# Optimization experiments

Measured on AMD Instinct MI355X. Metric: run time of the kernel, lower is better.

Reference implementation:

```python
import math
import jax, jax.numpy as jnp
import numpy as np

NUM_HEADS = 16
NEG_INF = -1e30


def setup_inputs() -> dict:
    key = jax.random.key(0)
    k1, k2, k3, k4 = jax.random.split(key, 4)
    B, C, T = 4, 1024, 2048
    x = jax.random.normal(k1, (B, C, T), dtype=jnp.float32)
    mask = jax.random.randint(k2, (B, T), 0, 2, dtype=jnp.int32)
    # kernel-size-1 Conv1d with bias=False == matmul; torch init scale ~ 1/sqrt(fan_in)
    W_mem = jax.random.normal(k3, (2 * C, C), dtype=jnp.float32) / math.sqrt(C)
    W_q = jax.random.normal(k4, (C, C), dtype=jnp.float32) / math.sqrt(C)
    return {"x": x, "mask": mask, "W_mem": W_mem, "W_q": W_q}


def reference(x, mask, W_mem, W_q):
    B, C, T = x.shape
    nh = NUM_HEADS
    dh = C // nh
    # kernel-size-1 conv projections, output already transposed to [B, T, ch]
    memory = jnp.einsum('oc,bct->bto', W_mem, x)   # [B, T, 2C]
    query = jnp.einsum('oc,bct->bto', W_q, x)      # [B, T, C]
    Q = query.reshape(B, T, nh, dh).transpose(0, 2, 1, 3)           # [B, nh, T, dh]
    Km, Vm = jnp.split(memory, 2, axis=-1)
    K = Km.reshape(B, T, nh, dh).transpose(0, 2, 1, 3)              # [B, nh, T, dh]
    V = Vm.reshape(B, T, nh, dh).transpose(0, 2, 1, 3)              # [B, nh, T, dh]
    att = jnp.einsum('bhqd,bhkd->bhqk', Q, K) * (1.0 / math.sqrt(dh))
    m = mask.reshape(B, 1, 1, T).astype(att.dtype)
    logits = m * att + (1.0 - m) * NEG_INF  # masked_softmax convention
    weights = jax.nn.softmax(logits, axis=-1)
    # dropout is identity in eval mode
    out = jnp.einsum('bhqk,bhkd->bhqd', weights, V)                 # [B, nh, T, dh]
    return out.transpose(0, 2, 1, 3).reshape(B, T, C).transpose(0, 2, 1)  # [B, C, T]
```

## Files before the change

kernel.cpp:

```cpp
#include <hip/hip_runtime.h>

#define B_ 4
#define C_ 1024
#define T_ 2048
#define NH 16
#define DH 64
#define TC 3072

typedef __attribute__((ext_vector_type(8))) short short8;
typedef __attribute__((ext_vector_type(4))) short short4v;
typedef __attribute__((ext_vector_type(4))) float f32x4;
typedef __attribute__((ext_vector_type(16))) float f32x16;
typedef __attribute__((ext_vector_type(2))) unsigned int u32x2;
typedef __attribute__((ext_vector_type(4))) unsigned int u32x4;

#define S2Q 0.1803368801111204f

static __device__ __forceinline__ unsigned short f2bf(float f){
  unsigned int u = __builtin_bit_cast(unsigned int, f);
  u += 0x7fffu + ((u >> 16) & 1u);
  return (unsigned short)(u >> 16);
}

__global__ __launch_bounds__(256) void cast_w_kernel(const float* __restrict__ Wmem,
                                                     const float* __restrict__ Wq,
                                                     unsigned short* __restrict__ Wc){
  size_t base = ((size_t)blockIdx.x*256 + threadIdx.x)*4;
  float4 v;
  if (base < (size_t)2048*1024) v = *(const float4*)(Wmem + base);
  else                          v = *(const float4*)(Wq + (base - (size_t)2048*1024));
  short4v o;
  o.x = (short)f2bf(v.x); o.y = (short)f2bf(v.y);
  o.z = (short)f2bf(v.z); o.w = (short)f2bf(v.w);
  *(short4v*)(Wc + base) = o;
}

__global__ __launch_bounds__(256) void scan_mask_kernel(const int* __restrict__ mask,
    int* __restrict__ idx, int* __restrict__ nkinfo, float* __restrict__ cbias){
  __shared__ int cnt[256];
  int b = blockIdx.x;
  int tid = threadIdx.x;
  const int* mb = mask + (size_t)b*T_;
  int base = tid*8;
  int m[8]; int c = 0;
  #pragma unroll
  for (int i=0;i<8;i++){ m[i] = mb[base+i]; c += m[i]; }
  cnt[tid] = c;
  __syncthreads();
  for (int off=1; off<256; off<<=1){
    int v = (tid >= off) ? cnt[tid-off] : 0;
    __syncthreads();
    cnt[tid] += v;
    __syncthreads();
  }
  int nk  = cnt[255];
  int pos = cnt[tid] - c;
  #pragma unroll
  for (int i=0;i<8;i++){
    if (m[i]) idx[(size_t)b*T_ + (pos++)] = base + i;
  }
  #pragma unroll
  for (int i=0;i<8;i++){
    int j = base + i;
    cbias[(size_t)b*T_ + j] = (j < nk) ? 0.f : -1e30f;
  }
  if (tid == 0){
    nkinfo[b]   = (nk + 127) & ~127;
    nkinfo[4+b] = nk;
  }
}

__global__ __launch_bounds__(256) void transpose_x_kernel(const float* __restrict__ x,
                                                          unsigned short* __restrict__ xT){
  __shared__ float tile[32][33];
  int b = blockIdx.z;
  int c0 = blockIdx.y*32, t0 = blockIdx.x*32;
  int tx = threadIdx.x, ty = threadIdx.y;
  const float* xp = x + ((size_t)b*C_ + c0)*T_ + t0;
  #pragma unroll
  for (int i=0;i<4;i++) tile[ty+8*i][tx] = xp[(size_t)(ty+8*i)*T_ + tx];
  __syncthreads();
  unsigned short* op = xT + ((size_t)b*T_ + t0)*C_ + c0;
  int cp = tx & 15, tw = tx >> 4;
  #pragma unroll
  for (int i=0;i<2;i++){
    int trow = ty + 8*tw + 16*i;
    unsigned int pk = (unsigned int)f2bf(tile[2*cp][trow])
                    | ((unsigned int)f2bf(tile[2*cp+1][trow]) << 16);
    *(unsigned int*)(op + (size_t)trow*C_ + 2*cp) = pk;
  }
}

#define PBM 128
#define PBN 128
#define PBK 64

__global__ __launch_bounds__(256) void proj_gemm_kernel(const unsigned short* __restrict__ Wc,
    const unsigned short* __restrict__ xT, const int* __restrict__ idx,
    const int* __restrict__ nkinfo,
    unsigned short* __restrict__ Kb, unsigned short* __restrict__ Vt,
    unsigned short* __restrict__ Qb){
  __shared__ unsigned short sA[PBM*PBK];
  __shared__ unsigned short sB[PBN*PBK];
  int b = blockIdx.y;
  int d = blockIdx.x;
  int xcd = d & 7, j = d >> 3;
  int oq = xcd >> 1, th = xcd & 1;
  int o0 = (oq*6 + (j % 6)) * PBM;
  int t0 = ((j/6)*2 + th) * PBN;
  const bool isKV = (o0 < 2*C_);
  const int nk128 = nkinfo[b], nk = nkinfo[4+b];
  if (isKV && t0 >= nk128) return;
  int tid = threadIdx.x;
  int lane = tid & 63, wave = tid >> 6;
  int wr = wave >> 1, wc = wave & 1;
  f32x4 acc[4][4] = {};
  const unsigned short* Abase = Wc + (size_t)o0*C_;
  const unsigned short* xTb = xT + (size_t)b*T_*C_;
  auto ldsA = (__attribute__((address_space(3))) char*)sA;
  auto ldsB = (__attribute__((address_space(3))) char*)sB;
  const char* srcBrow[4];
  #pragma unroll
  for (int i=0;i<4;i++){
    int L  = wave*4096 + i*1024;
    int Ll = L + lane*16;
    int row = Ll >> 7;
    int jb  = Ll & 127;
    int trow = t0 + row;
    int grow = trow;
    if (isKV) grow = (trow < nk) ? idx[(size_t)b*T_ + trow] : 0;
    srcBrow[i] = (const char*)(xTb + (size_t)grow*C_) + jb;
  }
  for (int k0=0; k0<C_; k0+=PBK){
    #pragma unroll
    for (int i=0;i<4;i++){
      int L  = wave*4096 + i*1024;
      int Ll = L + lane*16;
      int row = Ll >> 7;
      int jb  = Ll & 127;
      const char* srcA = (const char*)(Abase + (size_t)row*C_ + k0) + jb;
      const char* srcB = srcBrow[i] + (size_t)k0*2;
      __builtin_amdgcn_global_load_lds((const __attribute__((address_space(1))) void*)srcA,
                                       (__attribute__((address_space(3))) void*)(ldsA + L), 16, 0, 0);
      __builtin_amdgcn_global_load_lds((const __attribute__((address_space(1))) void*)srcB,
                                       (__attribute__((address_space(3))) void*)(ldsB + L), 16, 0, 0);
    }
    __syncthreads();
    #pragma unroll
    for (int ks=0; ks<2; ks++){
      short8 af[4], bfr[4];
      #pragma unroll
      for (int m=0;m<4;m++){
        int row = wr*64 + m*16 + (lane & 15);
        af[m] = *(const short8*)((const char*)sA + row*128 + ks*64 + ((lane>>4)*16));
      }
      #pragma unroll
      for (int n=0;n<4;n++){
        int row = wc*64 + n*16 + (lane & 15);
        bfr[n] = *(const short8*)((const char*)sB + row*128 + ks*64 + ((lane>>4)*16));
      }
      #pragma unroll
      for (int m=0;m<4;m++){
        #pragma unroll
        for (int n=0;n<4;n++)
          acc[m][n] = __builtin_amdgcn_mfma_f32_16x16x32_bf16(af[m], bfr[n], acc[m][n], 0, 0, 0);
      }
    }
    __syncthreads();
  }
  int rowbase = o0 + wr*64;
  #pragma unroll
  for (int m=0;m<4;m++){
    int o = rowbase + m*16 + ((lane>>4)*4);
    #pragma unroll
    for (int n=0;n<4;n++){
      int t = t0 + wc*64 + n*16 + (lane & 15);
      f32x4 v = acc[m][n];
      if (o < C_){
        int h = o >> 6, dd = o & 63;
        unsigned short* p = Kb + (((size_t)(b*NH + h)*T_ + t)*DH + dd);
        short4v s; s.x=(short)f2bf(v.x); s.y=(short)f2bf(v.y);
        s.z=(short)f2bf(v.z); s.w=(short)f2bf(v.w);
        *(short4v*)p = s;
      } else if (o < 2*C_){
        int oo = o - C_;
        int h = oo >> 6, dd = oo & 63;
        unsigned short* p = Vt + (((size_t)(b*NH + h)*DH + dd)*T_ + t);
        p[0]    = f2bf(v.x);
        p[T_]   = f2bf(v.y);
        p[2*T_] = f2bf(v.z);
        p[3*T_] = f2bf(v.w);
      } else {
        int oo = o - 2*C_;
        int h = oo >> 6, dd = oo & 63;
        unsigned short* p = Qb + (((size_t)(b*NH + h)*T_ + t)*DH + dd);
        short4v s; s.x=(short)f2bf(v.x*S2Q); s.y=(short)f2bf(v.y*S2Q);
        s.z=(short)f2bf(v.z*S2Q); s.w=(short)f2bf(v.w*S2Q);
        *(short4v*)p = s;
      }
    }
  }
}

#define KB_ 64

#define GLL(SRC, SHBUF, LOFF) \
  __builtin_amdgcn_global_load_lds((const __attribute__((address_space(1))) void*)(SRC), \
      (__attribute__((address_space(3))) void*)((__attribute__((address_space(3))) char*)(SHBUF) + (LOFF)), 16, 0, 0)

#define MAX3(a,b,c) fmaxf(fmaxf((a),(b)),(c))

__global__ __launch_bounds__(256) void attn_kernel(const unsigned short* __restrict__ Qb,
    const unsigned short* __restrict__ Kb, const unsigned short* __restrict__ Vt,
    const float* __restrict__ cbias, const int* __restrict__ nkinfo,
    float* __restrict__ out){
  __shared__ unsigned short sK[2][KB_*DH];
  __shared__ unsigned short sV[2][KB_*DH];
  const int Lid = blockIdx.x;
  const int xcd = Lid & 7, jj = Lid >> 3;
  const int bh = ((jj & 7) << 3) | xcd;
  const int qblk = jj >> 3;
  const int b = bh >> 4;
  const int ntiles = nkinfo[b] >> 6;
  const int tid = threadIdx.x, lane = tid & 63, wave = tid >> 6;
  const int l31 = lane & 31, h = lane >> 5;
  const int rsw = l31 & 7;
  const unsigned short* Kbase = Kb + (size_t)bh*T_*DH;
  const unsigned short* Vbase = Vt + (size_t)bh*DH*T_;
  const float* bptr = cbias + (size_t)b*T_ + 4*h;
  const int qrow = qblk*128 + wave*32 + l31;
  const unsigned short* Qp = Qb + ((size_t)bh*T_ + qrow)*DH + h*8;
  short8 qf[4];
  #pragma unroll
  for (int kc=0;kc<4;kc++) qf[kc] = *(const short8*)(Qp + kc*16);
  f32x16 acco0 = {}, acco1 = {};
  float mrun = -1e30f, lpart = 0.f;
  const int L0  = wave*2048;
  const int Ll0 = L0 + lane*16, Ll1 = Ll0 + 1024;
  const int row0 = Ll0 >> 7, row1 = Ll1 >> 7;
  const int cg0 = ((Ll0 >> 4) & 7) ^ (row0 & 7);
  const int cg1 = ((Ll1 >> 4) & 7) ^ (row1 & 7);
  const char* srcK0 = (const char*)Kbase + row0*128 + cg0*16;
  const char* srcK1 = (const char*)Kbase + row1*128 + cg1*16;
  const char* srcV0 = (const char*)Vbase + (size_t)row0*(T_*2) + cg0*16;
  const char* srcV1 = (const char*)Vbase + (size_t)row1*(T_*2) + cg1*16;

  GLL(srcK0, &sK[0][0], L0);
  GLL(srcK1, &sK[0][0], L0 + 1024);
  GLL(srcV0, &sV[0][0], L0);
  GLL(srcV1, &sV[0][0], L0 + 1024);
  srcK0 += 8192; srcK1 += 8192; srcV0 += 128; srcV1 += 128;
  __syncthreads();

  for (int kt = 0; kt < ntiles; kt++){
    const int cb = kt & 1;
    union { f32x4 q[4]; f32x16 v; } cb0, cb1;
    #pragma unroll
    for (int m=0;m<4;m++){
      cb0.q[m] = *(const f32x4*)(bptr + m*8);
      cb1.q[m] = *(const f32x4*)(bptr + 32 + m*8);
    }
    bptr += 64;
    if (kt + 1 < ntiles){
      int db = cb ^ 1;
      GLL(srcK0, &sK[0][0], db*8192 + L0);
      GLL(srcK1, &sK[0][0], db*8192 + L0 + 1024);
      GLL(srcV0, &sV[0][0], db*8192 + L0);
      GLL(srcV1, &sV[0][0], db*8192 + L0 + 1024);
      srcK0 += 8192; srcK1 += 8192; srcV0 += 128; srcV1 += 128;
      asm volatile("s_waitcnt vmcnt(12)" ::: "memory");
    } else {
      asm volatile("s_waitcnt vmcnt(8)" ::: "memory");
    }
    __builtin_amdgcn_s_barrier();
    __builtin_amdgcn_sched_barrier(0);
    const char* sKb = (const char*)&sK[0][0] + cb*8192 + l31*128;
    const char* sVb = (const char*)&sV[0][0] + cb*8192 + l31*128;
    f32x16 s0 = cb0.v, s1 = cb1.v;
    #pragma unroll
    for (int kc=0;kc<4;kc++){
      int co = (((kc<<1)|h) ^ rsw) << 4;
      short8 kf0 = *(const short8*)(sKb + co);
      short8 kf1 = *(const short8*)(sKb + 4096 + co);
      s0 = __builtin_amdgcn_mfma_f32_32x32x16_bf16(kf0, qf[kc], s0, 0,0,0);
      s1 = __builtin_amdgcn_mfma_f32_32x32x16_bf16(kf1, qf[kc], s1, 0,0,0);
    }
    float t0_ = MAX3(s0[0],s0[1],s0[2]),   t1_ = MAX3(s0[3],s0[4],s0[5]);
    float t2_ = MAX3(s0[6],s0[7],s0[8]),   t3_ = MAX3(s0[9],s0[10],s0[11]);
    float t4_ = MAX3(s0[12],s0[13],s0[14]), t5_ = MAX3(s0[15],s1[0],s1[1]);
    float t6_ = MAX3(s1[2],s1[3],s1[4]),   t7_ = MAX3(s1[5],s1[6],s1[7]);
    float t8_ = MAX3(s1[8],s1[9],s1[10]),  t9_ = MAX3(s1[11],s1[12],s1[13]);
    float u0_ = MAX3(t0_,t1_,t2_), u1_ = MAX3(t3_,t4_,t5_);
    float u2_ = MAX3(t6_,t7_,t8_), u3_ = MAX3(t9_,s1[14],s1[15]);
    float pmax = MAX3(MAX3(u0_,u1_,u2_), u3_, -1e30f);
    if (!__all(pmax - mrun <= 8.0f)){
      float pm = fmaxf(pmax, __shfl_xor(pmax, 32));
      float mnew = fmaxf(mrun, pm);
      float alpha = __builtin_amdgcn_exp2f(mrun - mnew);
      mrun = mnew; lpart *= alpha;
      #pragma unroll
      for (int r=0;r<16;r++){
        float ar = __shfl(alpha, (r&3) + 8*(r>>2) + 4*h);
        acco0[r] *= ar; acco1[r] *= ar;
      }
    }
    float ps_ = 0.f;
    #pragma unroll
    for (int j=0;j<16;j++){
      s0[j] = __builtin_amdgcn_exp2f(s0[j] - mrun); ps_ += s0[j];
      s1[j] = __builtin_amdgcn_exp2f(s1[j] - mrun); ps_ += s1[j];
    }
    lpart += ps_;
    unsigned int Wp[2][4][2];
    #pragma unroll
    for (int m=0;m<4;m++){
      asm volatile("v_cvt_pk_bf16_f32 %0, %1, %2" : "=v"(Wp[0][m][0]) : "v"(s0[4*m]),   "v"(s0[4*m+1]));
      asm volatile("v_cvt_pk_bf16_f32 %0, %1, %2" : "=v"(Wp[0][m][1]) : "v"(s0[4*m+2]), "v"(s0[4*m+3]));
      asm volatile("v_cvt_pk_bf16_f32 %0, %1, %2" : "=v"(Wp[1][m][0]) : "v"(s1[4*m]),   "v"(s1[4*m+1]));
      asm volatile("v_cvt_pk_bf16_f32 %0, %1, %2" : "=v"(Wp[1][m][1]) : "v"(s1[4*m+2]), "v"(s1[4*m+3]));
    }
    #pragma unroll
    for (int kb=0;kb<2;kb++){
      #pragma unroll
      for (int e=0;e<2;e++){
        u32x2 x0 = __builtin_amdgcn_permlane32_swap(Wp[kb][2*e][0], Wp[kb][2*e+1][0], 0, 0);
        u32x2 x1 = __builtin_amdgcn_permlane32_swap(Wp[kb][2*e][1], Wp[kb][2*e+1][1], 0, 0);
        u32x4 pw; pw.x = x0.x; pw.y = x1.x; pw.z = x0.y; pw.w = x1.y;
        short8 pf = __builtin_bit_cast(short8, pw);
        int vo = (((((kb<<1)|e)<<1)|h) ^ rsw) << 4;
        short8 vf0 = *(const short8*)(sVb + vo);
        short8 vf1 = *(const short8*)(sVb + 4096 + vo);
        acco0 = __builtin_amdgcn_mfma_f32_32x32x16_bf16(pf, vf0, acco0, 0,0,0);
        acco1 = __builtin_amdgcn_mfma_f32_32x32x16_bf16(pf, vf1, acco1, 0,0,0);
      }
    }
    __builtin_amdgcn_sched_barrier(0);
    __builtin_amdgcn_s_barrier();
  }

  lpart += __shfl_xor(lpart, 32);
  float inv = 1.0f / lpart;
  const int head = bh & 15;
  const int qbase = qblk*128 + wave*32;
  #pragma unroll
  for (int m=0;m<4;m++){
    float rv[4];
    #pragma unroll
    for (int s=0;s<4;s++) rv[s] = __shfl(inv, 8*m + 4*h + s);
    int t = qbase + 8*m + 4*h;
    float4 v0, v1;
    v0.x = acco0[4*m+0]*rv[0]; v0.y = acco0[4*m+1]*rv[1];
    v0.z = acco0[4*m+2]*rv[2]; v0.w = acco0[4*m+3]*rv[3];
    v1.x = acco1[4*m+0]*rv[0]; v1.y = acco1[4*m+1]*rv[1];
    v1.z = acco1[4*m+2]*rv[2]; v1.w = acco1[4*m+3]*rv[3];
    size_t off0 = ((size_t)b*C_ + head*64 + l31)*T_ + t;
    size_t off1 = ((size_t)b*C_ + head*64 + 32 + l31)*T_ + t;
    *(float4*)(out + off0) = v0;
    *(float4*)(out + off1) = v1;
  }
}

extern "C" void kernel_launch(void* const* d_in, const int* in_sizes, int n_in,
                              void* d_out, int out_size, void* d_ws, size_t ws_size,
                              hipStream_t stream) {
  const float* x    = (const float*)d_in[0];
  const int*   mask = (const int*)d_in[1];
  const float* Wmem = (const float*)d_in[2];
  const float* Wq   = (const float*)d_in[3];
  float* out = (float*)d_out;

  unsigned short* ws = (unsigned short*)d_ws;
  unsigned short* xT = ws;
  unsigned short* Wc = xT + (size_t)B_*T_*C_;
  unsigned short* Qb = Wc + (size_t)TC*C_;
  unsigned short* Kb = Qb + (size_t)B_*NH*T_*DH;
  unsigned short* Vt = Kb + (size_t)B_*NH*T_*DH;
  float* cbias = (float*)(Vt + (size_t)B_*NH*T_*DH);
  int*   idx   = (int*)(cbias + (size_t)B_*T_);
  int*   nkinfo = idx + (size_t)B_*T_;

  cast_w_kernel<<<dim3(TC*C_/1024), dim3(256), 0, stream>>>(Wmem, Wq, Wc);
  scan_mask_kernel<<<dim3(B_), dim3(256), 0, stream>>>(mask, idx, nkinfo, cbias);
  transpose_x_kernel<<<dim3(T_/32, C_/32, B_), dim3(32,8), 0, stream>>>(x, xT);
  proj_gemm_kernel<<<dim3((TC/PBM)*(T_/PBN), B_), dim3(256), 0, stream>>>(Wc, xT, idx, nkinfo, Kb, Vt, Qb);
  attn_kernel<<<dim3((T_/128)*(B_*NH)), dim3(256), 0, stream>>>(Qb, Kb, Vt, cbias, nkinfo, out);
}
```

Baseline: 165.6 us.

## Double-buffer LDS tiles in projection GEMM to overlap loads with MFMA

The projection GEMM now uses two LDS buffers for the A and B tiles. It issues async global-to-LDS loads for the next K slice before computing on the current one, using a manual vmcnt wait and raw barriers in place of the two __syncthreads per iteration. This is meant to hide global memory latency behind MFMA work. In exchange, LDS use doubles to 64KB per block, which may lower occupancy, and correctness now depends on the hand-written waitcnt count.

```diff
diff --git a/kernel.cpp b/kernel.cpp
--- a/kernel.cpp
+++ b/kernel.cpp
@@ -100,8 +100,8 @@
     const int* __restrict__ nkinfo,
     unsigned short* __restrict__ Kb, unsigned short* __restrict__ Vt,
     unsigned short* __restrict__ Qb){
-  __shared__ unsigned short sA[PBM*PBK];
-  __shared__ unsigned short sB[PBN*PBK];
+  __shared__ unsigned short sA[2][PBM*PBK];
+  __shared__ unsigned short sB[2][PBN*PBK];
   int b = blockIdx.y;
   int d = blockIdx.x;
   int xcd = d & 7, j = d >> 3;
@@ -117,47 +117,63 @@
   f32x4 acc[4][4] = {};
   const unsigned short* Abase = Wc + (size_t)o0*C_;
   const unsigned short* xTb = xT + (size_t)b*T_*C_;
-  auto ldsA = (__attribute__((address_space(3))) char*)sA;
-  auto ldsB = (__attribute__((address_space(3))) char*)sB;
+  auto ldsA = (__attribute__((address_space(3))) char*)&sA[0][0];
+  auto ldsB = (__attribute__((address_space(3))) char*)&sB[0][0];
+  const int L  = wave*4096;
+  const int Ll = L + lane*16;
+  const int srow = Ll >> 7;
+  const int sjb  = Ll & 127;
   const char* srcBrow[4];
+  const char* srcArow[4];
   #pragma unroll
   for (int i=0;i<4;i++){
-    int L  = wave*4096 + i*1024;
-    int Ll = L + lane*16;
-    int row = Ll >> 7;
-    int jb  = Ll & 127;
+    int row = srow + i*8;
     int trow = t0 + row;
     int grow = trow;
     if (isKV) grow = (trow < nk) ? idx[(size_t)b*T_ + trow] : 0;
-    srcBrow[i] = (const char*)(xTb + (size_t)grow*C_) + jb;
-  }
-  for (int k0=0; k0<C_; k0+=PBK){
-    #pragma unroll
-    for (int i=0;i<4;i++){
-      int L  = wave*4096 + i*1024;
-      int Ll = L + lane*16;
-      int row = Ll >> 7;
-      int jb  = Ll & 127;
-      const char* srcA = (const char*)(Abase + (size_t)row*C_ + k0) + jb;
-      const char* srcB = srcBrow[i] + (size_t)k0*2;
-      __builtin_amdgcn_global_load_lds((const __attribute__((address_space(1))) void*)srcA,
-                                       (__attribute__((address_space(3))) void*)(ldsA + L), 16, 0, 0);
-      __builtin_amdgcn_global_load_lds((const __attribute__((address_space(1))) void*)srcB,
-                                       (__attribute__((address_space(3))) void*)(ldsB + L), 16, 0, 0);
-    }
-    __syncthreads();
+    srcBrow[i] = (const char*)(xTb + (size_t)grow*C_) + sjb;
+    srcArow[i] = (const char*)(Abase + (size_t)row*C_) + sjb;
+  }
+
+#define PSTAGE(BF, K0) do {                                                            \
+    _Pragma("unroll")                                                                  \
+    for (int i=0;i<4;i++){                                                             \
+      __builtin_amdgcn_global_load_lds(                                                \
+        (const __attribute__((address_space(1))) void*)(srcArow[i] + (size_t)(K0)*2),  \
+        (__attribute__((address_space(3))) void*)(ldsA + (BF)*16384 + L + i*1024), 16, 0, 0); \
+      __builtin_amdgcn_global_load_lds(                                                \
+        (const __attribute__((address_space(1))) void*)(srcBrow[i] + (size_t)(K0)*2),  \
+        (__attribute__((address_space(3))) void*)(ldsB + (BF)*16384 + L + i*1024), 16, 0, 0); \
+    }                                                                                  \
+  } while(0)
+
+  PSTAGE(0, 0);
+  __syncthreads();
+
+  for (int kk=0; kk<C_/PBK; kk++){
+    int bf = kk & 1;
+    if (kk + 1 < C_/PBK){
+      PSTAGE(bf^1, (kk+1)*PBK);
+      asm volatile("s_waitcnt vmcnt(8)" ::: "memory");
+    } else {
+      asm volatile("s_waitcnt vmcnt(0)" ::: "memory");
+    }
+    __builtin_amdgcn_s_barrier();
+    __builtin_amdgcn_sched_barrier(0);
+    const char* sAb = (const char*)&sA[bf][0];
+    const char* sBb = (const char*)&sB[bf][0];
     #pragma unroll
     for (int ks=0; ks<2; ks++){
       short8 af[4], bfr[4];
       #pragma unroll
       for (int m=0;m<4;m++){
         int row = wr*64 + m*16 + (lane & 15);
-        af[m] = *(const short8*)((const char*)sA + row*128 + ks*64 + ((lane>>4)*16));
+        af[m] = *(const short8*)(sAb + row*128 + ks*64 + ((lane>>4)*16));
       }
       #pragma unroll
       for (int n=0;n<4;n++){
         int row = wc*64 + n*16 + (lane & 15);
-        bfr[n] = *(const short8*)((const char*)sB + row*128 + ks*64 + ((lane>>4)*16));
+        bfr[n] = *(const short8*)(sBb + row*128 + ks*64 + ((lane>>4)*16));
       }
       #pragma unroll
       for (int m=0;m<4;m++){
@@ -166,8 +182,11 @@
           acc[m][n] = __builtin_amdgcn_mfma_f32_16x16x32_bf16(af[m], bfr[n], acc[m][n], 0, 0, 0);
       }
     }
-    __syncthreads();
-  }
+    __builtin_amdgcn_sched_barrier(0);
+    __builtin_amdgcn_s_barrier();
+  }
+#undef PSTAGE
+
   int rowbase = o0 + wr*64;
   #pragma unroll
   for (int m=0;m<4;m++){
```

Measured after the change: 165.8 us. No clear change (+0.1%).

## Project all K/V rows densely, then compact unmasked keys in a separate kernel

Applied to the files above, without the earlier changes.

The projection GEMM no longer gathers unmasked time rows through an index array and no longer skips tiles past the unmasked count. It computes K and V for every position. A new kernel then gathers the unmasked rows into compacted K/V buffers for attention. This gives simpler, contiguous GEMM loads in exchange for roughly double the K/V GEMM work, an extra launch, and scattered scalar gathers for the transposed V.

```diff
diff --git a/kernel.cpp b/kernel.cpp
--- a/kernel.cpp
+++ b/kernel.cpp
@@ -96,8 +96,7 @@
 #define PBK 64
 
 __global__ __launch_bounds__(256) void proj_gemm_kernel(const unsigned short* __restrict__ Wc,
-    const unsigned short* __restrict__ xT, const int* __restrict__ idx,
-    const int* __restrict__ nkinfo,
+    const unsigned short* __restrict__ xT,
     unsigned short* __restrict__ Kb, unsigned short* __restrict__ Vt,
     unsigned short* __restrict__ Qb){
   __shared__ unsigned short sA[PBM*PBK];
@@ -108,29 +107,14 @@
   int oq = xcd >> 1, th = xcd & 1;
   int o0 = (oq*6 + (j % 6)) * PBM;
   int t0 = ((j/6)*2 + th) * PBN;
-  const bool isKV = (o0 < 2*C_);
-  const int nk128 = nkinfo[b], nk = nkinfo[4+b];
-  if (isKV && t0 >= nk128) return;
   int tid = threadIdx.x;
   int lane = tid & 63, wave = tid >> 6;
   int wr = wave >> 1, wc = wave & 1;
   f32x4 acc[4][4] = {};
   const unsigned short* Abase = Wc + (size_t)o0*C_;
-  const unsigned short* xTb = xT + (size_t)b*T_*C_;
+  const unsigned short* Bbase = xT + ((size_t)b*T_ + t0)*C_;
   auto ldsA = (__attribute__((address_space(3))) char*)sA;
   auto ldsB = (__attribute__((address_space(3))) char*)sB;
-  const char* srcBrow[4];
-  #pragma unroll
-  for (int i=0;i<4;i++){
-    int L  = wave*4096 + i*1024;
-    int Ll = L + lane*16;
-    int row = Ll >> 7;
-    int jb  = Ll & 127;
-    int trow = t0 + row;
-    int grow = trow;
-    if (isKV) grow = (trow < nk) ? idx[(size_t)b*T_ + trow] : 0;
-    srcBrow[i] = (const char*)(xTb + (size_t)grow*C_) + jb;
-  }
   for (int k0=0; k0<C_; k0+=PBK){
     #pragma unroll
     for (int i=0;i<4;i++){
@@ -139,7 +123,7 @@
       int row = Ll >> 7;
       int jb  = Ll & 127;
       const char* srcA = (const char*)(Abase + (size_t)row*C_ + k0) + jb;
-      const char* srcB = srcBrow[i] + (size_t)k0*2;
+      const char* srcB = (const char*)(Bbase + (size_t)row*C_ + k0) + jb;
       __builtin_amdgcn_global_load_lds((const __attribute__((address_space(1))) void*)srcA,
                                        (__attribute__((address_space(3))) void*)(ldsA + L), 16, 0, 0);
       __builtin_amdgcn_global_load_lds((const __attribute__((address_space(1))) void*)srcB,
@@ -202,6 +186,49 @@
   }
 }
 
+__global__ __launch_bounds__(256) void compact_kv_kernel(const unsigned short* __restrict__ KbF,
+    const unsigned short* __restrict__ VtF, const int* __restrict__ idx,
+    const int* __restrict__ nkinfo,
+    unsigned short* __restrict__ Kc, unsigned short* __restrict__ Vc){
+  int bh = blockIdx.y;
+  int b = bh >> 4;
+  int nk128 = nkinfo[b], nk = nkinfo[4+b];
+  int tid = threadIdx.x;
+  int row = blockIdx.x*32 + (tid >> 3);
+  if (row < nk128){
+    int col = (tid & 7)*8;
+    const unsigned short* s;
+    short8 v;
+    if (row < nk){
+      int g = idx[(size_t)b*T_ + row];
+      v = *(const short8*)(KbF + ((size_t)bh*T_ + g)*DH + col);
+    } else {
+      v = short8{};
+    }
+    *(short8*)(Kc + ((size_t)bh*T_ + row)*DH + col) = v;
+  }
+  for (int it=0; it<2; it++){
+    int dd = blockIdx.x;
+    if (dd < DH){
+      int jj = (tid + it*256)*4;
+      if (jj < nk128){
+        short4v v;
+        #pragma unroll
+        for (int u=0;u<4;u++){
+          int j2 = jj + u;
+          unsigned short val = 0;
+          if (j2 < nk){
+            int g = idx[(size_t)b*T_ + j2];
+            val = VtF[((size_t)bh*DH + dd)*T_ + g];
+          }
+          ((unsigned short*)&v)[u] = val;
+        }
+        *(short4v*)(Vc + ((size_t)bh*DH + dd)*T_ + jj) = v;
+      }
+    }
+  }
+}
+
 #define KB_ 64
 
 #define GLL(SRC, SHBUF, LOFF) \
@@ -378,10 +405,13 @@
   float* cbias = (float*)(Vt + (size_t)B_*NH*T_*DH);
   int*   idx   = (int*)(cbias + (size_t)B_*T_);
   int*   nkinfo = idx + (size_t)B_*T_;
+  unsigned short* Kc = (unsigned short*)(nkinfo + 8);
+  unsigned short* Vc = Kc + (size_t)B_*NH*T_*DH;
 
   cast_w_kernel<<<dim3(TC*C_/1024), dim3(256), 0, stream>>>(Wmem, Wq, Wc);
   scan_mask_kernel<<<dim3(B_), dim3(256), 0, stream>>>(mask, idx, nkinfo, cbias);
   transpose_x_kernel<<<dim3(T_/32, C_/32, B_), dim3(32,8), 0, stream>>>(x, xT);
-  proj_gemm_kernel<<<dim3((TC/PBM)*(T_/PBN), B_), dim3(256), 0, stream>>>(Wc, xT, idx, nkinfo, Kb, Vt, Qb);
-  attn_kernel<<<dim3((T_/128)*(B_*NH)), dim3(256), 0, stream>>>(Qb, Kb, Vt, cbias, nkinfo, out);
-}
+  proj_gemm_kernel<<<dim3((TC/PBM)*(T_/PBN), B_), dim3(256), 0, stream>>>(Wc, xT, Kb, Vt, Qb);
+  compact_kv_kernel<<<dim3(T_/32, B_*NH), dim3(256), 0, stream>>>(Kb, Vt, idx, nkinfo, Kc, Vc);
+  attn_kernel<<<dim3((T_/128)*(B_*NH)), dim3(256), 0, stream>>>(Qb, Kc, Vc, cbias, nkinfo, out);
+}
```

Result: slower. 179.4 us (+8.3%).

## Use persistent 256x128 projection GEMM tiles with 512 threads and compacted tile list

Applied to the files above, without the earlier changes.

The projection GEMM switches to a persistent grid of 128 blocks per batch with 512 threads, each looping over a compacted list of 256x128 output tiles. Only Q tiles and the key/value tiles below the masked key count are visited. The change aims to cut grid-launch waste from early-exit blocks and to raise operand reuse per loaded B tile. The trade-off is larger LDS use per block, fewer resident blocks, and possible load imbalance across the persistent loop. The XCD-aware tile swizzle is removed.

```diff
diff --git a/kernel.cpp b/kernel.cpp
--- a/kernel.cpp
+++ b/kernel.cpp
@@ -91,114 +91,118 @@
   }
 }
 
-#define PBM 128
+#define PBM 256
 #define PBN 128
 #define PBK 64
 
-__global__ __launch_bounds__(256) void proj_gemm_kernel(const unsigned short* __restrict__ Wc,
+__global__ __launch_bounds__(512) void proj_gemm_kernel(const unsigned short* __restrict__ Wc,
     const unsigned short* __restrict__ xT, const int* __restrict__ idx,
     const int* __restrict__ nkinfo,
     unsigned short* __restrict__ Kb, unsigned short* __restrict__ Vt,
     unsigned short* __restrict__ Qb){
   __shared__ unsigned short sA[PBM*PBK];
   __shared__ unsigned short sB[PBN*PBK];
-  int b = blockIdx.y;
-  int d = blockIdx.x;
-  int xcd = d & 7, j = d >> 3;
-  int oq = xcd >> 1, th = xcd & 1;
-  int o0 = (oq*6 + (j % 6)) * PBM;
-  int t0 = ((j/6)*2 + th) * PBN;
-  const bool isKV = (o0 < 2*C_);
+  const int b = blockIdx.y;
+  const int d = blockIdx.x;
   const int nk128 = nkinfo[b], nk = nkinfo[4+b];
-  if (isKV && t0 >= nk128) return;
-  int tid = threadIdx.x;
-  int lane = tid & 63, wave = tid >> 6;
-  int wr = wave >> 1, wc = wave & 1;
-  f32x4 acc[4][4] = {};
-  const unsigned short* Abase = Wc + (size_t)o0*C_;
+  const int L = 64 + 8*(nk128 >> 7);
+  const int tid = threadIdx.x;
+  const int lane = tid & 63, wave = tid >> 6;
+  const int wr = wave >> 1, wc = wave & 1;
   const unsigned short* xTb = xT + (size_t)b*T_*C_;
   auto ldsA = (__attribute__((address_space(3))) char*)sA;
   auto ldsB = (__attribute__((address_space(3))) char*)sB;
-  const char* srcBrow[4];
-  #pragma unroll
-  for (int i=0;i<4;i++){
-    int L  = wave*4096 + i*1024;
-    int Ll = L + lane*16;
-    int row = Ll >> 7;
-    int jb  = Ll & 127;
-    int trow = t0 + row;
-    int grow = trow;
-    if (isKV) grow = (trow < nk) ? idx[(size_t)b*T_ + trow] : 0;
-    srcBrow[i] = (const char*)(xTb + (size_t)grow*C_) + jb;
-  }
-  for (int k0=0; k0<C_; k0+=PBK){
-    #pragma unroll
-    for (int i=0;i<4;i++){
-      int L  = wave*4096 + i*1024;
-      int Ll = L + lane*16;
-      int row = Ll >> 7;
-      int jb  = Ll & 127;
-      const char* srcA = (const char*)(Abase + (size_t)row*C_ + k0) + jb;
-      const char* srcB = srcBrow[i] + (size_t)k0*2;
-      __builtin_amdgcn_global_load_lds((const __attribute__((address_space(1))) void*)srcA,
-                                       (__attribute__((address_space(3))) void*)(ldsA + L), 16, 0, 0);
-      __builtin_amdgcn_global_load_lds((const __attribute__((address_space(1))) void*)srcB,
-                                       (__attribute__((address_space(3))) void*)(ldsB + L), 16, 0, 0);
+  const int l15 = lane & 15, lg4 = (lane >> 4)*16;
+
+  for (int i = d; i < L; i += 128){
+    int o0, t0;
+    bool isKV;
+    if (i < 64){ o0 = 2048 + (i >> 4)*PBM; t0 = (i & 15)*PBN; isKV = false; }
+    else       { int k = i - 64; o0 = (k & 7)*PBM; t0 = (k >> 3)*PBN; isKV = true; }
+    const unsigned short* Abase = Wc + (size_t)o0*C_;
+    f32x4 acc[4][4] = {};
+    const char* srcBrow[2];
+    #pragma unroll
+    for (int i2=0;i2<2;i2++){
+      int Ll = wave*2048 + i2*1024 + lane*16;
+      int row = Ll >> 7, jb = Ll & 127;
+      int t = t0 + row;
+      int grow = isKV ? ((t < nk) ? idx[(size_t)b*T_ + t] : 0) : t;
+      srcBrow[i2] = (const char*)(xTb + (size_t)grow*C_) + jb;
+    }
+    for (int k0=0; k0<C_; k0+=PBK){
+      #pragma unroll
+      for (int i2=0;i2<4;i2++){
+        int Lb = wave*4096 + i2*1024;
+        int Ll = Lb + lane*16;
+        int row = Ll >> 7, jb = Ll & 127;
+        const char* srcA = (const char*)(Abase + (size_t)row*C_ + k0) + jb;
+        __builtin_amdgcn_global_load_lds((const __attribute__((address_space(1))) void*)srcA,
+                                         (__attribute__((address_space(3))) void*)(ldsA + Lb), 16, 0, 0);
+      }
+      #pragma unroll
+      for (int i2=0;i2<2;i2++){
+        int Lb = wave*2048 + i2*1024;
+        const char* srcB = srcBrow[i2] + (size_t)k0*2;
+        __builtin_amdgcn_global_load_lds((const __attribute__((address_space(1))) void*)srcB,
+                                         (__attribute__((address_space(3))) void*)(ldsB + Lb), 16, 0, 0);
+      }
+      __syncthreads();
+      #pragma unroll
+      for (int ks=0; ks<2; ks++){
+        short8 af[4], bfr[4];
+        #pragma unroll
+        for (int m=0;m<4;m++){
+          int row = wr*64 + m*16 + l15;
+          af[m] = *(const short8*)((const char*)sA + row*128 + ks*64 + lg4);
+        }
+        #pragma unroll
+        for (int n=0;n<4;n++){
+          int row = wc*64 + n*16 + l15;
+          bfr[n] = *(const short8*)((const char*)sB + row*128 + ks*64 + lg4);
+        }
+        #pragma unroll
+        for (int m=0;m<4;m++){
+          #pragma unroll
+          for (int n=0;n<4;n++)
+            acc[m][n] = __builtin_amdgcn_mfma_f32_16x16x32_bf16(af[m], bfr[n], acc[m][n], 0, 0, 0);
+        }
+      }
+      __syncthreads();
+    }
+    int rowbase = o0 + wr*64;
+    #pragma unroll
+    for (int m=0;m<4;m++){
+      int o = rowbase + m*16 + ((lane>>4)*4);
+      #pragma unroll
+      for (int n=0;n<4;n++){
+        int t = t0 + wc*64 + n*16 + l15;
+        f32x4 v = acc[m][n];
+        if (o < C_){
+          int h = o >> 6, dd = o & 63;
+          unsigned short* p = Kb + (((size_t)(b*NH + h)*T_ + t)*DH + dd);
+          short4v s; s.x=(short)f2bf(v.x); s.y=(short)f2bf(v.y);
+          s.z=(short)f2bf(v.z); s.w=(short)f2bf(v.w);
+          *(short4v*)p = s;
+        } else if (o < 2*C_){
+          int oo = o - C_;
+          int h = oo >> 6, dd = oo & 63;
+          unsigned short* p = Vt + (((size_t)(b*NH + h)*DH + dd)*T_ + t);
+          p[0]    = f2bf(v.x);
+          p[T_]   = f2bf(v.y);
+          p[2*T_] = f2bf(v.z);
+          p[3*T_] = f2bf(v.w);
+        } else {
+          int oo = o - 2*C_;
+          int h = oo >> 6, dd = oo & 63;
+          unsigned short* p = Qb + (((size_t)(b*NH + h)*T_ + t)*DH + dd);
+          short4v s; s.x=(short)f2bf(v.x*S2Q); s.y=(short)f2bf(v.y*S2Q);
+          s.z=(short)f2bf(v.z*S2Q); s.w=(short)f2bf(v.w*S2Q);
+          *(short4v*)p = s;
+        }
+      }
     }
     __syncthreads();
-    #pragma unroll
-    for (int ks=0; ks<2; ks++){
-      short8 af[4], bfr[4];
-      #pragma unroll
-      for (int m=0;m<4;m++){
-        int row = wr*64 + m*16 + (lane & 15);
-        af[m] = *(const short8*)((const char*)sA + row*128 + ks*64 + ((lane>>4)*16));
-      }
-      #pragma unroll
-      for (int n=0;n<4;n++){
-        int row = wc*64 + n*16 + (lane & 15);
-        bfr[n] = *(const short8*)((const char*)sB + row*128 + ks*64 + ((lane>>4)*16));
-      }
-      #pragma unroll
-      for (int m=0;m<4;m++){
-        #pragma unroll
-        for (int n=0;n<4;n++)
-          acc[m][n] = __builtin_amdgcn_mfma_f32_16x16x32_bf16(af[m], bfr[n], acc[m][n], 0, 0, 0);
-      }
-    }
-    __syncthreads();
-  }
-  int rowbase = o0 + wr*64;
-  #pragma unroll
-  for (int m=0;m<4;m++){
-    int o = rowbase + m*16 + ((lane>>4)*4);
-    #pragma unroll
-    for (int n=0;n<4;n++){
-      int t = t0 + wc*64 + n*16 + (lane & 15);
-      f32x4 v = acc[m][n];
-      if (o < C_){
-        int h = o >> 6, dd = o & 63;
-        unsigned short* p = Kb + (((size_t)(b*NH + h)*T_ + t)*DH + dd);
-        short4v s; s.x=(short)f2bf(v.x); s.y=(short)f2bf(v.y);
-        s.z=(short)f2bf(v.z); s.w=(short)f2bf(v.w);
-        *(short4v*)p = s;
-      } else if (o < 2*C_){
-        int oo = o - C_;
-        int h = oo >> 6, dd = oo & 63;
-        unsigned short* p = Vt + (((size_t)(b*NH + h)*DH + dd)*T_ + t);
-        p[0]    = f2bf(v.x);
-        p[T_]   = f2bf(v.y);
-        p[2*T_] = f2bf(v.z);
-        p[3*T_] = f2bf(v.w);
-      } else {
-        int oo = o - 2*C_;
-        int h = oo >> 6, dd = oo & 63;
-        unsigned short* p = Qb + (((size_t)(b*NH + h)*T_ + t)*DH + dd);
-        short4v s; s.x=(short)f2bf(v.x*S2Q); s.y=(short)f2bf(v.y*S2Q);
-        s.z=(short)f2bf(v.z*S2Q); s.w=(short)f2bf(v.w*S2Q);
-        *(short4v*)p = s;
-      }
-    }
   }
 }
 
@@ -382,6 +386,6 @@
   cast_w_kernel<<<dim3(TC*C_/1024), dim3(256), 0, stream>>>(Wmem, Wq, Wc);
   scan_mask_kernel<<<dim3(B_), dim3(256), 0, stream>>>(mask, idx, nkinfo, cbias);
   transpose_x_kernel<<<dim3(T_/32, C_/32, B_), dim3(32,8), 0, stream>>>(x, xT);
-  proj_gemm_kernel<<<dim3((TC/PBM)*(T_/PBN), B_), dim3(256), 0, stream>>>(Wc, xT, idx, nkinfo, Kb, Vt, Qb);
+  proj_gemm_kernel<<<dim3(128, B_), dim3(512), 0, stream>>>(Wc, xT, idx, nkinfo, Kb, Vt, Qb);
   attn_kernel<<<dim3((T_/128)*(B_*NH)), dim3(256), 0, stream>>>(Qb, Kb, Vt, cbias, nkinfo, out);
 }
```

After: 182.3 us. 10.1% more time.
